# Kernel optimization log

Hardware: AMD Instinct MI355X
Metric: run time of the kernel (lower is better)

## Reference

```python
import jax, jax.numpy as jnp
import numpy as np

N_VERTEX = 16384
D_IN = 128
D_OUT = 128
N_REGIONS = 64


def setup_inputs() -> dict:
    key = jax.random.key(0)
    k1, k2, k3, k4, k5 = jax.random.split(key, 5)
    h = jax.random.normal(k1, (N_VERTEX, D_IN), dtype=jnp.float32)
    # row-normalized-ish dense adjacency (small positive entries)
    norm_adj = jax.random.uniform(k2, (N_VERTEX, N_VERTEX), dtype=jnp.float32) / N_VERTEX
    region_index = jax.random.randint(k3, (N_VERTEX,), 0, N_REGIONS, dtype=jnp.int64)
    weight = jax.random.normal(k4, (D_IN, D_OUT), dtype=jnp.float32) / np.sqrt(D_IN)
    lag_weight = jax.random.normal(k5, (D_IN, D_OUT), dtype=jnp.float32) / np.sqrt(D_IN)
    reg_param = jnp.ones((N_REGIONS, D_IN), dtype=jnp.float32)
    bias = jnp.zeros((D_OUT,), dtype=jnp.float32)
    return {"h": h, "norm_adj": norm_adj, "region_index": region_index,
            "weight": weight, "lag_weight": lag_weight,
            "reg_param": reg_param, "bias": bias}


def reference(h, norm_adj, region_index, weight, lag_weight, reg_param, bias):
    # per-vertex region gather (vectorized) + elementwise mul
    reg_weight = reg_param[region_index]            # [N, d_in]
    rwh = h * reg_weight                            # [N, d_in]
    ra = rwh @ weight                               # [N, d_out]
    rb = norm_adj @ (rwh @ lag_weight)              # [N, d_out]
    return ra + rb + bias
```

## Files before the change

kernel.cpp:

```cpp
#include <hip/hip_runtime.h>
#include <hip/hip_bf16.h>

#define NV 16384
#define DD 128

typedef __attribute__((ext_vector_type(8))) short bf16x8;
typedef __attribute__((ext_vector_type(8))) unsigned short ushort8v;
typedef __attribute__((ext_vector_type(4))) float f32x4;
typedef __attribute__((ext_vector_type(2))) int i32x2;
typedef long long i64;

#define ASCALE 16384.0f
#define INV_ASCALE (1.0f / 16384.0f)

__device__ __forceinline__ unsigned short f2bf(float x) {
  unsigned u = __builtin_bit_cast(unsigned, x);
  u = (u + 0x7FFFu + ((u >> 16) & 1u)) >> 16;
  return (unsigned short)u;
}

__device__ __forceinline__ i64 pk8(f32x4 a, f32x4 b, float s) {
  int lo = 0, hi = 0;
  lo = __builtin_amdgcn_cvt_pk_fp8_f32(a[0] * s, a[1] * s, lo, false);
  lo = __builtin_amdgcn_cvt_pk_fp8_f32(a[2] * s, a[3] * s, lo, true);
  hi = __builtin_amdgcn_cvt_pk_fp8_f32(b[0] * s, b[1] * s, hi, false);
  hi = __builtin_amdgcn_cvt_pk_fp8_f32(b[2] * s, b[3] * s, hi, true);
  i32x2 r; r[0] = lo; r[1] = hi;
  return __builtin_bit_cast(i64, r);
}

__global__ __launch_bounds__(256) void k_small(
    const float* __restrict__ h, const long long* __restrict__ ridx,
    const float* __restrict__ W, const float* __restrict__ LW,
    const float* __restrict__ RP, const float* __restrict__ bias,
    float* __restrict__ ws_ra, i32x2* __restrict__ tT8)
{
  __shared__ unsigned short rw [64 * 128];
  __shared__ unsigned short Wts[128 * 128];
  __shared__ unsigned short LWts[128 * 128];
  const int tid = threadIdx.x;
  const int r0  = blockIdx.x * 64;

  {
    const int k  = tid >> 1;
    const int j0 = (tid & 1) * 64;
    const float* wr  = W  + k * DD + j0;
    const float* lwr = LW + k * DD + j0;
#pragma unroll 8
    for (int i = 0; i < 64; ++i) {
      const int j = j0 + i;
      const int off = j * 128 + (((k >> 3) ^ (j & 7)) << 3) + (k & 7);
      Wts [off] = f2bf(wr[i]);
      LWts[off] = f2bf(lwr[i]);
    }
  }

  {
    const int r  = tid >> 2;
    const int cc = tid & 3;
    const int v  = r0 + r;
    const int reg = ((int)ridx[v]) & 63;
    const float* hp = h  + (size_t)v * DD + cc * 32;
    const float* rp = RP + reg * DD + cc * 32;
#pragma unroll
    for (int i = 0; i < 4; ++i) {
      const f32x4 a  = *(const f32x4*)(hp + i * 8);
      const f32x4 b  = *(const f32x4*)(hp + i * 8 + 4);
      const f32x4 pa = *(const f32x4*)(rp + i * 8);
      const f32x4 pb = *(const f32x4*)(rp + i * 8 + 4);
      ushort8v pk;
#pragma unroll
      for (int q = 0; q < 4; ++q) {
        pk[q]     = f2bf(a[q] * pa[q]);
        pk[4 + q] = f2bf(b[q] * pb[q]);
      }
      const int sc = (cc * 4 + i) ^ (r & 7);
      *(ushort8v*)&rw[r * 128 + sc * 8] = pk;
    }
  }
  __syncthreads();

  const int w = tid >> 6, lane = tid & 63, g = lane >> 4, l15 = lane & 15;
  f32x4 accA[8], accT[8];
#pragma unroll
  for (int f = 0; f < 8; ++f) {
    accA[f] = (f32x4){0.f, 0.f, 0.f, 0.f};
    accT[f] = (f32x4){0.f, 0.f, 0.f, 0.f};
  }
  const int arow = w * 16 + l15;
#pragma unroll
  for (int s = 0; s < 4; ++s) {
    const int sca = (s * 4 + g) ^ (l15 & 7);
    const bf16x8 af = *(const bf16x8*)&rw[arow * 128 + sca * 8];
#pragma unroll
    for (int f = 0; f < 8; ++f) {
      const int j = f * 16 + l15;
      const int scb = (s * 4 + g) ^ (l15 & 7);
      const bf16x8 bw = *(const bf16x8*)&Wts [j * 128 + scb * 8];
      accA[f] = __builtin_amdgcn_mfma_f32_16x16x32_bf16(af, bw, accA[f], 0, 0, 0);
      const bf16x8 bl = *(const bf16x8*)&LWts[j * 128 + scb * 8];
      accT[f] = __builtin_amdgcn_mfma_f32_16x16x32_bf16(af, bl, accT[f], 0, 0, 0);
    }
  }

#pragma unroll
  for (int f = 0; f < 8; ++f) {
    const int col = f * 16 + l15;
    const float bj = bias[col];
#pragma unroll
    for (int q = 0; q < 4; ++q) {
      const int v = r0 + w * 16 + g * 4 + q;
      ws_ra[(size_t)v * DD + col] = accA[f][q] + bj;
    }
  }
#pragma unroll
  for (int f = 0; f < 8; ++f) {
    const int j = f * 16 + l15;
    int own = 0;
    own = __builtin_amdgcn_cvt_pk_fp8_f32(accT[f][0], accT[f][1], own, false);
    own = __builtin_amdgcn_cvt_pk_fp8_f32(accT[f][2], accT[f][3], own, true);
    const int partner = __shfl_xor(own, 16, 64);
    if ((g & 1) == 0) {
      const int v0 = r0 + w * 16 + g * 4;
      i32x2 val; val[0] = own; val[1] = partner;
      tT8[(v0 >> 6) * 1024 + ((v0 >> 3) & 7) * 128 + j] = val;
    }
  }
}

__global__ __launch_bounds__(256, 2) void k_big(
    const float* __restrict__ adj, const unsigned char* __restrict__ tTb,
    float* __restrict__ part)
{
  __shared__ unsigned char Bs[3][24576] __attribute__((aligned(16)));
  const int tid  = threadIdx.x;
  const int w    = tid >> 6;
  const int lane = tid & 63;
  const int g    = lane >> 4;
  const int l15  = lane & 15;
  const int hb   = blockIdx.x;
  const int kh   = (hb & 7) >> 2;
  const int mblk = (hb >> 3) * 4 + (hb & 3);
  const int bid  = mblk * 2 + kh;
  const int r0   = mblk * 64;
  const int t0   = mblk & 127;
  const unsigned char* bbase = tTb + (size_t)kh * 128 * 8192;

#define RT(t) ((t0 + (t)) & 127)

  const float* asrc[4];
#pragma unroll
  for (int i = 0; i < 4; ++i) {
    const int rrel = w * 16 + i * 4 + (lane >> 4);
    const int cswz = (lane & 15) ^ ((i * 4 + (lane >> 4)) & 7);
    asrc[i] = adj + (size_t)(r0 + rrel) * NV + kh * (NV / 2) + cswz * 4;
  }

  f32x4 acc[8];
#pragma unroll
  for (int f = 0; f < 8; ++f) acc[f] = (f32x4){0.f, 0.f, 0.f, 0.f};

#define STAGE(bufidx, rt) do {                                                 \
    _Pragma("unroll")                                                          \
    for (int i_ = 0; i_ < 4; ++i_) {      \
      const float* srcA_ = asrc[i_] + (size_t)(rt) * 64;                       \
      unsigned char* dstA_ = &Bs[bufidx][(w * 16 + i_ * 4) * 256];             \
      __builtin_amdgcn_global_load_lds(                                        \
          (const __attribute__((address_space(1))) unsigned int*)srcA_,        \
          (__attribute__((address_space(3))) unsigned int*)dstA_, 16, 0, 0);   \
    }                                                                          \
    _Pragma("unroll")                                                          \
    for (int i_ = 0; i_ < 2; ++i_) {                          \
      const int unit_ = i_ * 4 + w;                                            \
      const unsigned char* srcB_ = bbase + (size_t)(rt) * 8192 +               \
                                   unit_ * 1024 + lane * 16;                   \
      unsigned char* dstB_ = &Bs[bufidx][16384 + unit_ * 1024];                \
      __builtin_amdgcn_global_load_lds(                                        \
          (const __attribute__((address_space(1))) unsigned int*)srcB_,        \
          (__attribute__((address_space(3))) unsigned int*)dstB_, 16, 0, 0);   \
    } } while (0)

#define COMP(bufidx) do {                                                      \
    const unsigned char* Ab_ = &Bs[bufidx][(w * 16 + l15) * 256];              \
    const int x_ = l15 & 7;                                                    \
    const f32x4 c0_ = *(const f32x4*)&Ab_[((2 * g)     ^ x_) * 16];            \
    const f32x4 c1_ = *(const f32x4*)&Ab_[((2 * g + 1) ^ x_) * 16];            \
    const f32x4 c2_ = *(const f32x4*)&Ab_[((8 + 2 * g)     ^ x_) * 16];        \
    const f32x4 c3_ = *(const f32x4*)&Ab_[((8 + 2 * g + 1) ^ x_) * 16];        \
    const i64 a0_ = pk8(c0_, c1_, ASCALE);                                     \
    const i64 a1_ = pk8(c2_, c3_, ASCALE);                                     \
    const unsigned char* Bb_ = &Bs[bufidx][16384];                             \
    _Pragma("unroll")                                                          \
    for (int f_ = 0; f_ < 8; ++f_) {                                           \
      const int jr8_ = (f_ * 16 + l15) * 8;                                    \
      acc[f_] = __builtin_amdgcn_mfma_f32_16x16x32_fp8_fp8(a0_,                \
          *(const i64*)&Bb_[g * 1024 + jr8_],       acc[f_], 0, 0, 0);         \
      acc[f_] = __builtin_amdgcn_mfma_f32_16x16x32_fp8_fp8(a1_,                \
          *(const i64*)&Bb_[(4 + g) * 1024 + jr8_], acc[f_], 0, 0, 0);         \
    } } while (0)

#define VW6  asm volatile("s_waitcnt vmcnt(6)" ::: "memory")
#define VW0  asm volatile("s_waitcnt vmcnt(0)" ::: "memory")
#define BAR  __builtin_amdgcn_s_barrier()

  STAGE(0, RT(0));
  STAGE(1, RT(1));

  for (int tq = 0; tq < 42; ++tq) {
    const int t = tq * 3;
    VW6; BAR; STAGE(2, RT(t + 2)); COMP(0);
    VW6; BAR; STAGE(0, RT(t + 3)); COMP(1);
    VW6; BAR; STAGE(1, RT(t + 4)); COMP(2);
  }
  VW6; BAR; COMP(0);
  VW0; BAR; COMP(1);

#undef STAGE
#undef COMP
#undef VW6
#undef VW0
#undef BAR
#undef RT

  float* pbase = part + ((size_t)bid * 64 + w * 16) * DD;
#pragma unroll
  for (int f = 0; f < 8; ++f) {
    const int col = f * 16 + l15;
#pragma unroll
    for (int q = 0; q < 4; ++q) {
      const int row = g * 4 + q;
      pbase[row * DD + col] = acc[f][q];
    }
  }
}

__global__ __launch_bounds__(256) void k_reduce(
    const float* __restrict__ part, const float* __restrict__ ws_ra,
    float* __restrict__ out)
{
  const size_t e = ((size_t)blockIdx.x * 256 + threadIdx.x) * 4;
  const int    mblk  = (int)(e >> 13);
  const int    local = (int)(e & 8191);
  const f32x4 p0 = *(const f32x4*)&part[(size_t)(2 * mblk)     * 8192 + local];
  const f32x4 p1 = *(const f32x4*)&part[(size_t)(2 * mblk + 1) * 8192 + local];
  const f32x4 ra = *(const f32x4*)&ws_ra[e];
  f32x4 o;
#pragma unroll
  for (int i = 0; i < 4; ++i) o[i] = (p0[i] + p1[i]) * INV_ASCALE + ra[i];
  *(f32x4*)&out[e] = o;
}

extern "C" void kernel_launch(void* const* d_in, const int* in_sizes, int n_in,
                              void* d_out, int out_size, void* d_ws, size_t ws_size,
                              hipStream_t stream) {
  const float*     h    = (const float*)d_in[0];
  const float*     adj  = (const float*)d_in[1];
  const long long* ridx = (const long long*)d_in[2];
  const float*     W    = (const float*)d_in[3];
  const float*     LW   = (const float*)d_in[4];
  const float*     RP   = (const float*)d_in[5];
  const float*     bias = (const float*)d_in[6];
  float* out = (float*)d_out;

  float* ws_ra = (float*)d_ws;
  void*  tT8   = (void*)((char*)d_ws + (size_t)8  * 1024 * 1024);
  float* part  = (float*)((char*)d_ws + (size_t)16 * 1024 * 1024);

  hipLaunchKernelGGL(k_small, dim3(NV / 64), dim3(256), 0, stream,
                     h, ridx, W, LW, RP, bias, ws_ra, (i32x2*)tT8);
  hipLaunchKernelGGL(k_big, dim3(NV / 64 * 2), dim3(256), 0, stream,
                     adj, (const unsigned char*)tT8, part);
  hipLaunchKernelGGL(k_reduce, dim3((NV * DD / 4) / 256), dim3(256), 0, stream,
                     part, ws_ra, out);
}
```

Measured before the change: 218.9 us.

## Fuse split-K reduction into big GEMM kernel via atomic completion flags

Removes the separate reduce kernel. Each pair of split-K blocks increments a per-row-block counter, and the second block to finish adds its in-register accumulator to its partner's partial, then applies the scale and the ra term before writing the output. This saves one kernel launch and one full read and write pass over the partials. In exchange it adds a thread fence, an atomic and a partial-buffer round trip at the end of each block, and it relies on k_small resetting the flags on every call.

```diff
diff --git a/kernel.cpp b/kernel.cpp
--- a/kernel.cpp
+++ b/kernel.cpp
@@ -33,13 +33,16 @@
     const float* __restrict__ h, const long long* __restrict__ ridx,
     const float* __restrict__ W, const float* __restrict__ LW,
     const float* __restrict__ RP, const float* __restrict__ bias,
-    float* __restrict__ ws_ra, i32x2* __restrict__ tT8)
+    float* __restrict__ ws_ra, i32x2* __restrict__ tT8,
+    int* __restrict__ flags)
 {
   __shared__ unsigned short rw [64 * 128];
   __shared__ unsigned short Wts[128 * 128];
   __shared__ unsigned short LWts[128 * 128];
   const int tid = threadIdx.x;
   const int r0  = blockIdx.x * 64;
+
+  if (tid == 0) flags[blockIdx.x] = 0;
 
   {
     const int k  = tid >> 1;
@@ -130,9 +133,11 @@
 
 __global__ __launch_bounds__(256, 2) void k_big(
     const float* __restrict__ adj, const unsigned char* __restrict__ tTb,
-    float* __restrict__ part)
+    const float* __restrict__ ws_ra, float* __restrict__ part,
+    int* __restrict__ flags, float* __restrict__ out)
 {
   __shared__ unsigned char Bs[3][24576] __attribute__((aligned(16)));
+  __shared__ int s_old;
   const int tid  = threadIdx.x;
   const int w    = tid >> 6;
   const int lane = tid & 63;
@@ -232,22 +237,28 @@
       pbase[row * DD + col] = acc[f][q];
     }
   }
-}
-
-__global__ __launch_bounds__(256) void k_reduce(
-    const float* __restrict__ part, const float* __restrict__ ws_ra,
-    float* __restrict__ out)
-{
-  const size_t e = ((size_t)blockIdx.x * 256 + threadIdx.x) * 4;
-  const int    mblk  = (int)(e >> 13);
-  const int    local = (int)(e & 8191);
-  const f32x4 p0 = *(const f32x4*)&part[(size_t)(2 * mblk)     * 8192 + local];
-  const f32x4 p1 = *(const f32x4*)&part[(size_t)(2 * mblk + 1) * 8192 + local];
-  const f32x4 ra = *(const f32x4*)&ws_ra[e];
-  f32x4 o;
-#pragma unroll
-  for (int i = 0; i < 4; ++i) o[i] = (p0[i] + p1[i]) * INV_ASCALE + ra[i];
-  *(f32x4*)&out[e] = o;
+  __threadfence();
+  __syncthreads();
+  if (tid == 0) s_old = atomicAdd(&flags[mblk], 1);
+  __syncthreads();
+  if (s_old == 1) {
+    __threadfence();
+    const int pbid = mblk * 2 + (kh ^ 1);
+    const float* qbase  = part  + ((size_t)pbid * 64 + w * 16) * DD;
+    const float* rabase = ws_ra + (size_t)(r0 + w * 16) * DD;
+    float*       obase  = out   + (size_t)(r0 + w * 16) * DD;
+#pragma unroll
+    for (int f = 0; f < 8; ++f) {
+      const int col = f * 16 + l15;
+#pragma unroll
+      for (int q = 0; q < 4; ++q) {
+        const int row = g * 4 + q;
+        obase[row * DD + col] =
+            (acc[f][q] + qbase[row * DD + col]) * INV_ASCALE +
+            rabase[row * DD + col];
+      }
+    }
+  }
 }
 
 extern "C" void kernel_launch(void* const* d_in, const int* in_sizes, int n_in,
@@ -265,11 +276,10 @@
   float* ws_ra = (float*)d_ws;
   void*  tT8   = (void*)((char*)d_ws + (size_t)8  * 1024 * 1024);
   float* part  = (float*)((char*)d_ws + (size_t)16 * 1024 * 1024);
+  int*   flags = (int*)((char*)d_ws + (size_t)32 * 1024 * 1024);
 
   hipLaunchKernelGGL(k_small, dim3(NV / 64), dim3(256), 0, stream,
-                     h, ridx, W, LW, RP, bias, ws_ra, (i32x2*)tT8);
+                     h, ridx, W, LW, RP, bias, ws_ra, (i32x2*)tT8, flags);
   hipLaunchKernelGGL(k_big, dim3(NV / 64 * 2), dim3(256), 0, stream,
-                     adj, (const unsigned char*)tT8, part);
-  hipLaunchKernelGGL(k_reduce, dim3((NV * DD / 4) / 256), dim3(256), 0, stream,
-                     part, ws_ra, out);
-}
+                     adj, (const unsigned char*)tT8, ws_ra, part, flags, out);
+}
```

Result: slower. 339.3 us (+55.0%).
